# Optimization experiments

Hardware: AMD Instinct MI355X
Metric: run time of the kernel (lower is better)

## Reference

```python
import jax, jax.numpy as jnp
import numpy as np

N = 100000          # nodes
E = 1600000         # edges (before self-loops)
D_IN = 128          # graph.x feature dim
D_HID = 8           # hidden_dim = output_dim = 8 (hard-coded in __init__)
NUM_MASK = 10000    # int(0.1 * N), _mask_rate = 0.1
ATT_SLOPE = 0.2     # GATConv attention LeakyReLU slope
ACT_SLOPE = 0.01    # F.leaky_relu default slope


def setup_inputs() -> dict:
    key = jax.random.key(0)
    ks = jax.random.split(key, 16)
    x = jax.random.normal(ks[0], (N, D_IN), dtype=jnp.float32)
    edge_index = jax.random.randint(ks[1], (2, E), 0, N, dtype=jnp.int32)
    mask_nodes = jax.random.permutation(ks[2], N)[:NUM_MASK].astype(jnp.int32)
    s = lambda k, shape: jax.random.normal(k, shape, dtype=jnp.float32) * 0.1
    return {
        "x": x,
        "edge_index": edge_index,
        "mask_nodes": mask_nodes,
        "enc_mask_token": jnp.zeros((1, D_IN), dtype=jnp.float32),
        "enc_W": s(ks[3], (D_HID, D_IN)),
        "enc_a_src": s(ks[4], (D_HID,)),
        "enc_a_dst": s(ks[5], (D_HID,)),
        "enc_b": s(ks[6], (D_HID,)),
        "e2d_W": s(ks[7], (D_HID, D_HID)),
        "dec_W": s(ks[8], (D_IN, D_HID)),
        "dec_a_src": s(ks[9], (D_IN,)),
        "dec_a_dst": s(ks[10], (D_IN,)),
        "dec_b": s(ks[11], (D_IN,)),
    }


def gat_conv(x, W, a_src, a_dst, b, src, dst, n_nodes):
    """PyG GATConv, heads=1 (self-loops already appended to src/dst)."""
    h = x @ W.T                                  # [N, out]
    alpha_src = h @ a_src                        # [N]
    alpha_dst = h @ a_dst                        # [N]
    e = jax.nn.leaky_relu(alpha_src[src] + alpha_dst[dst], ATT_SLOPE)  # [E]
    # numerically-stable segment softmax over incoming edges per dst node
    m = jax.ops.segment_max(e, dst, num_segments=n_nodes)
    ex = jnp.exp(e - m[dst])
    denom = jax.ops.segment_sum(ex, dst, num_segments=n_nodes)
    alpha = ex / denom[dst]                      # [E]
    out = jax.ops.segment_sum(alpha[:, None] * h[src], dst, num_segments=n_nodes)
    return out + b


def reference(x, edge_index, mask_nodes, enc_mask_token,
              enc_W, enc_a_src, enc_a_dst, enc_b,
              e2d_W, dec_W, dec_a_src, dec_a_dst, dec_b):
    n = x.shape[0]
    # GATConv adds self-loops internally
    loops = jnp.arange(n, dtype=edge_index.dtype)
    src = jnp.concatenate([edge_index[0], loops])
    dst = jnp.concatenate([edge_index[1], loops])

    # encoding_mask_noise: out_x[mask]=0 then += enc_mask_token -> set to token
    use_x = x.at[mask_nodes].set(enc_mask_token[0])

    # encoder: GATConv(input_dim -> 8) + leaky_relu
    enc_rep = jax.nn.leaky_relu(
        gat_conv(use_x, enc_W, enc_a_src, enc_a_dst, enc_b, src, dst, n), ACT_SLOPE)

    rep = enc_rep @ e2d_W.T
    rep = rep.at[mask_nodes].set(0.0)            # re-mask before decoding

    # decoder: GATConv(8 -> input_dim) + leaky_relu
    recon = jax.nn.leaky_relu(
        gat_conv(rep, dec_W, dec_a_src, dec_a_dst, dec_b, src, dst, n), ACT_SLOPE)

    # cosine reconstruction loss on masked nodes (torch eps = 1e-8)
    x_init = x[mask_nodes]
    x_rec = recon[mask_nodes]
    eps = jnp.float32(1e-8)
    na = jnp.maximum(jnp.linalg.norm(x_rec, axis=-1), eps)
    nb = jnp.maximum(jnp.linalg.norm(x_init, axis=-1), eps)
    cos = jnp.sum(x_rec * x_init, axis=-1) / (na * nb)
    loss = 1.0 - jnp.mean(cos)
    return loss, enc_rep
```

## Files before the change

### kernel.cpp

```cpp
#include <hip/hip_runtime.h>

#define N_NODES 100000
#define N_EDGES 1600000
#define D_IN    128
#define D_H     8
#define N_MASK  10000

#define TS      256
#define NTE     391
#define CAPB    5760
#define TSD     64
#define NTD     157
#define CAPD    1536
#define NB_NODE 196
#define EPB     2048
#define NB_BKT  782

__device__ __forceinline__ float lrelu(float v, float s){ return v > 0.f ? v : s*v; }

__device__ __forceinline__ float wave_sum(float v){
#pragma unroll
  for (int o = 32; o > 0; o >>= 1) v += __shfl_xor(v, o, 64);
  return v;
}

__global__ void k_init(int* __restrict__ mask_slot, int* __restrict__ gcur_enc,
                       int* __restrict__ gcur_dec, float* __restrict__ cos_sum,
                       int* __restrict__ ticket){
  int i = blockIdx.x*blockDim.x + threadIdx.x;
  if (i < N_NODES) mask_slot[i] = -1;
  if (i < NTE) gcur_enc[i] = 0;
  if (i < NTD) gcur_dec[i] = 0;
  if (i == 0){ cos_sum[0] = 0.f; ticket[0] = 0; }
}

__global__ void k_ms(const int* __restrict__ mask_nodes, int* __restrict__ mask_slot,
                     const float* __restrict__ Wd, const float* __restrict__ a_src,
                     float* __restrict__ vvec){
  int i = blockIdx.x*blockDim.x + threadIdx.x;
  if (i < N_MASK) mask_slot[mask_nodes[i]] = i;
  if (blockIdx.x == 0 && threadIdx.x < D_H){
    float s = 0.f;
    for (int j = 0; j < D_IN; ++j) s += a_src[j] * Wd[j*D_H + threadIdx.x];
    vvec[threadIdx.x] = s;
  }
}

__global__ void __launch_bounds__(512) k_pre(
    const float* __restrict__ x, const float* __restrict__ token,
    const float* __restrict__ W, const float* __restrict__ a_src,
    const float* __restrict__ a_dst, const int* __restrict__ mask_slot,
    const int* __restrict__ ei,
    float* __restrict__ h1, float* __restrict__ as1, float* __restrict__ ad1,
    int* __restrict__ gcur_enc, int* __restrict__ gcur_dec,
    unsigned* __restrict__ be, unsigned* __restrict__ bd){
  __shared__ int smem[1104];
  if (blockIdx.x < NB_NODE){
    float* Ws = (float*)smem;
    float* sa = Ws + D_H*D_IN;
    float* sd = sa + D_H;
    for (int t = threadIdx.x; t < D_H*D_IN; t += 512) Ws[t] = W[t];
    if (threadIdx.x < D_H)            sa[threadIdx.x] = a_src[threadIdx.x];
    else if (threadIdx.x < 2*D_H)     sd[threadIdx.x - D_H] = a_dst[threadIdx.x - D_H];
    __syncthreads();
    int wid = blockIdx.x*512 + threadIdx.x;
    if (wid >= N_NODES) return;
    const float* row = (mask_slot[wid] >= 0) ? token : (x + (size_t)wid*D_IN);
    float acc[D_H];
#pragma unroll
    for (int j = 0; j < D_H; ++j) acc[j] = 0.f;
#pragma unroll 8
    for (int i = 0; i < D_IN/4; ++i){
      float4 xc = *(const float4*)(row + 4*i);
#pragma unroll
      for (int j = 0; j < D_H; ++j){
        float4 wv = *(const float4*)(Ws + j*D_IN + 4*i);
        acc[j] += xc.x*wv.x + xc.y*wv.y + xc.z*wv.z + xc.w*wv.w;
      }
    }
    float as = 0.f, ad = 0.f;
#pragma unroll
    for (int j = 0; j < D_H; ++j){ as += acc[j]*sa[j]; ad += acc[j]*sd[j]; }
    float4* hp = (float4*)(h1 + (size_t)wid*D_H);
    hp[0] = make_float4(acc[0], acc[1], acc[2], acc[3]);
    hp[1] = make_float4(acc[4], acc[5], acc[6], acc[7]);
    as1[wid] = as; ad1[wid] = ad;
  } else {
    int* h_enc    = smem;
    int* base_enc = h_enc + NTE;
    int* h_dec    = base_enc + NTE;
    int* base_dec = h_dec + NTD;
    int tid = threadIdx.x;
    if (tid < NTE) h_enc[tid] = 0;
    if (tid < NTD) h_dec[tid] = 0;
    __syncthreads();
    int t0 = (blockIdx.x - NB_NODE)*EPB;
    int s[4], d[4], sl[4];
#pragma unroll
    for (int k = 0; k < 4; ++k){
      int t = t0 + tid + k*512;
      s[k] = -1;
      if (t < N_EDGES){
        s[k] = ei[t]; d[k] = ei[N_EDGES + t];
        sl[k] = mask_slot[d[k]];
        atomicAdd(&h_enc[d[k] >> 8], 1);
        if (sl[k] >= 0) atomicAdd(&h_dec[sl[k] >> 6], 1);
      }
    }
    __syncthreads();
    if (tid < NTE){ base_enc[tid] = atomicAdd(&gcur_enc[tid], h_enc[tid]); h_enc[tid] = 0; }
    if (tid < NTD){ base_dec[tid] = atomicAdd(&gcur_dec[tid], h_dec[tid]); h_dec[tid] = 0; }
    __syncthreads();
#pragma unroll
    for (int k = 0; k < 4; ++k){
      if (s[k] >= 0){
        int b = d[k] >> 8, loc = d[k] & 255;
        int idx = base_enc[b] + atomicAdd(&h_enc[b], 1);
        if (idx < CAPB) be[(size_t)b*CAPB + idx] = ((unsigned)s[k] << 8) | (unsigned)loc;
        if (sl[k] >= 0){
          int bs = sl[k] >> 6, locs = sl[k] & 63;
          int i2 = base_dec[bs] + atomicAdd(&h_dec[bs], 1);
          if (i2 < CAPD) bd[(size_t)bs*CAPD + i2] = ((unsigned)s[k] << 6) | (unsigned)locs;
        }
      }
    }
  }
}

__global__ void __launch_bounds__(512) k_agg_enc(const unsigned* __restrict__ be,
                          const int* __restrict__ gcur_enc,
                          const float* __restrict__ as1, const float* __restrict__ ad1,
                          const float* __restrict__ h1,
                          const float* __restrict__ enc_b, const float* __restrict__ e2dW,
                          const int* __restrict__ mask_slot, const float* __restrict__ v,
                          float* __restrict__ out_rep, float* __restrict__ rep,
                          float* __restrict__ ex2){
  __shared__ unsigned sorted[CAPB];
  __shared__ int hist[TS], off[TS], cur[TS];
  __shared__ float lad[TS];
  __shared__ float comb[TS*9];
  int tau = blockIdx.x, tid = threadIdx.x;
  int gb = tau*TS;
  if (tid < TS){
    hist[tid] = 0;
    int g = gb + tid; lad[tid] = (g < N_NODES) ? ad1[g] : 0.f;
  }
  __syncthreads();
  int n = min(gcur_enc[tau], CAPB);
  const unsigned* bb = be + (size_t)tau*CAPB;
  for (int i = tid; i < n; i += 512) atomicAdd(&hist[bb[i] & 255], 1);
  __syncthreads();
  if (tid < TS) off[tid] = hist[tid];
  __syncthreads();
#pragma unroll
  for (int s2 = 1; s2 < TS; s2 <<= 1){
    int vv = 0;
    if (tid < TS && tid >= s2) vv = off[tid - s2];
    __syncthreads();
    if (tid < TS) off[tid] += vv;
    __syncthreads();
  }
  if (tid < TS) cur[tid] = off[tid] - hist[tid];
  __syncthreads();
  for (int i = tid; i < n; i += 512){
    unsigned w = bb[i];
    int pos = atomicAdd(&cur[w & 255], 1);
    sorted[pos] = w;
  }
  __syncthreads();
  int c = tid & 255, half = tid >> 8;
  int start = off[c] - hist[c], deg = hist[c];
  int mid = start + ((deg + 1) >> 1), end = start + deg;
  int k0 = half ? mid : start, k1 = half ? end : mid;
  float adv = lad[c];
  float acc[9];
#pragma unroll
  for (int j = 0; j < 9; ++j) acc[j] = 0.f;
  auto edge1 = [&](unsigned w){
    int s = w >> 8;
    float as = as1[s];
    float4 ha = *(const float4*)(h1 + (size_t)s*D_H);
    float4 hb = *(const float4*)(h1 + (size_t)s*D_H + 4);
    float ex = __expf(lrelu(as + adv, 0.2f));
    acc[0] += ex*ha.x; acc[1] += ex*ha.y; acc[2] += ex*ha.z; acc[3] += ex*ha.w;
    acc[4] += ex*hb.x; acc[5] += ex*hb.y; acc[6] += ex*hb.z; acc[7] += ex*hb.w;
    acc[8] += ex;
  };
  int k = k0;
  for (; k + 4 <= k1; k += 4){
    unsigned w0 = sorted[k], w1 = sorted[k+1], w2 = sorted[k+2], w3 = sorted[k+3];
    int s0 = w0 >> 8, s1 = w1 >> 8, s2 = w2 >> 8, s3 = w3 >> 8;
    float a0 = as1[s0], a1 = as1[s1], a2 = as1[s2], a3 = as1[s3];
    float4 h0a = *(const float4*)(h1 + (size_t)s0*D_H), h0b = *(const float4*)(h1 + (size_t)s0*D_H + 4);
    float4 h1a = *(const float4*)(h1 + (size_t)s1*D_H), h1b = *(const float4*)(h1 + (size_t)s1*D_H + 4);
    float4 h2a = *(const float4*)(h1 + (size_t)s2*D_H), h2b = *(const float4*)(h1 + (size_t)s2*D_H + 4);
    float4 h3a = *(const float4*)(h1 + (size_t)s3*D_H), h3b = *(const float4*)(h1 + (size_t)s3*D_H + 4);
    float e0 = __expf(lrelu(a0 + adv, 0.2f));
    float e1 = __expf(lrelu(a1 + adv, 0.2f));
    float e2 = __expf(lrelu(a2 + adv, 0.2f));
    float e3 = __expf(lrelu(a3 + adv, 0.2f));
    acc[0] += e0*h0a.x + e1*h1a.x + e2*h2a.x + e3*h3a.x;
    acc[1] += e0*h0a.y + e1*h1a.y + e2*h2a.y + e3*h3a.y;
    acc[2] += e0*h0a.z + e1*h1a.z + e2*h2a.z + e3*h3a.z;
    acc[3] += e0*h0a.w + e1*h1a.w + e2*h2a.w + e3*h3a.w;
    acc[4] += e0*h0b.x + e1*h1b.x + e2*h2b.x + e3*h3b.x;
    acc[5] += e0*h0b.y + e1*h1b.y + e2*h2b.y + e3*h3b.y;
    acc[6] += e0*h0b.z + e1*h1b.z + e2*h2b.z + e3*h3b.z;
    acc[7] += e0*h0b.w + e1*h1b.w + e2*h2b.w + e3*h3b.w;
    acc[8] += e0 + e1 + e2 + e3;
  }
  for (; k < k1; ++k) edge1(sorted[k]);
  if (half){
#pragma unroll
    for (int j = 0; j < 9; ++j) comb[c*9 + j] = acc[j];
  }
  __syncthreads();
  if (!half){
    int i = gb + c;
    if (i < N_NODES){
#pragma unroll
      for (int j = 0; j < 9; ++j) acc[j] += comb[c*9 + j];
      {
        float exs = __expf(lrelu(as1[i] + adv, 0.2f));
        float4 ha = *(const float4*)(h1 + (size_t)i*D_H);
        float4 hb = *(const float4*)(h1 + (size_t)i*D_H + 4);
        acc[0] += exs*ha.x; acc[1] += exs*ha.y; acc[2] += exs*ha.z; acc[3] += exs*ha.w;
        acc[4] += exs*hb.x; acc[5] += exs*hb.y; acc[6] += exs*hb.z; acc[7] += exs*hb.w;
        acc[8] += exs;
      }
      float inv = 1.0f / acc[8];
      float er[D_H];
#pragma unroll
      for (int j = 0; j < D_H; ++j){
        er[j] = lrelu(acc[j]*inv + enc_b[j], 0.01f);
        out_rep[(size_t)i*D_H + j] = er[j];
      }
      bool masked = mask_slot[i] >= 0;
      float as = 0.f;
      float rv[D_H];
#pragma unroll
      for (int kk = 0; kk < D_H; ++kk){
        float t = 0.f;
#pragma unroll
        for (int j = 0; j < D_H; ++j) t += er[j]*e2dW[kk*D_H + j];
        t = masked ? 0.f : t;
        rv[kk] = t;
        as += t * v[kk];
      }
      float4* rp = (float4*)(rep + (size_t)i*D_H);
      rp[0] = make_float4(rv[0], rv[1], rv[2], rv[3]);
      rp[1] = make_float4(rv[4], rv[5], rv[6], rv[7]);
      ex2[i] = __expf(lrelu(as, 0.2f));
    }
  }
}

__global__ void __launch_bounds__(512) k_agg_dec(const unsigned* __restrict__ bd,
                          const int* __restrict__ gcur_dec,
                          const float* __restrict__ ex2, const float* __restrict__ rep,
                          const float* __restrict__ Wd, const float* __restrict__ dec_b,
                          const int* __restrict__ mask_nodes, const float* __restrict__ x,
                          float* __restrict__ cos_sum, int* __restrict__ ticket,
                          float* __restrict__ out){
  __shared__ unsigned sorted[CAPD];
  __shared__ int hist[TSD], off[TSD], cur[TSD];
  __shared__ float comb[TSD*9];
  __shared__ float Wt[D_H*D_IN];
  __shared__ float wsum[8];
  int sg = blockIdx.x, tid = threadIdx.x;
  if (tid < TSD) hist[tid] = 0;
  for (int t = tid; t < D_H*D_IN; t += 512) Wt[(t & 7)*D_IN + (t >> 3)] = Wd[t];
  __syncthreads();
  int n = min(gcur_dec[sg], CAPD);
  const unsigned* bb = bd + (size_t)sg*CAPD;
  for (int i = tid; i < n; i += 512) atomicAdd(&hist[bb[i] & 63], 1);
  __syncthreads();
  if (tid < TSD) off[tid] = hist[tid];
  __syncthreads();
#pragma unroll
  for (int s2 = 1; s2 < TSD; s2 <<= 1){
    int vv = 0;
    if (tid < TSD && tid >= s2) vv = off[tid - s2];
    __syncthreads();
    if (tid < TSD) off[tid] += vv;
    __syncthreads();
  }
  if (tid < TSD) cur[tid] = off[tid] - hist[tid];
  __syncthreads();
  for (int i = tid; i < n; i += 512){
    unsigned w = bb[i];
    int pos = atomicAdd(&cur[w & 63], 1);
    sorted[pos] = w;
  }
  __syncthreads();
  int c = tid >> 3, part = tid & 7;
  int start = off[c] - hist[c], deg = hist[c], end = start + deg;
  float acc[9];
#pragma unroll
  for (int j = 0; j < 9; ++j) acc[j] = 0.f;
  int k = start + part;
  for (; k + 8 < end; k += 16){
    unsigned w0 = sorted[k], w1 = sorted[k+8];
    int sA = w0 >> 6, sB = w1 >> 6;
    float eA = ex2[sA], eB = ex2[sB];
    float4 raA = *(const float4*)(rep + (size_t)sA*D_H);
    float4 rbA = *(const float4*)(rep + (size_t)sA*D_H + 4);
    float4 raB = *(const float4*)(rep + (size_t)sB*D_H);
    float4 rbB = *(const float4*)(rep + (size_t)sB*D_H + 4);
    acc[0] += eA*raA.x; acc[1] += eA*raA.y; acc[2] += eA*raA.z; acc[3] += eA*raA.w;
    acc[4] += eA*rbA.x; acc[5] += eA*rbA.y; acc[6] += eA*rbA.z; acc[7] += eA*rbA.w;
    acc[8] += eA;
    acc[0] += eB*raB.x; acc[1] += eB*raB.y; acc[2] += eB*raB.z; acc[3] += eB*raB.w;
    acc[4] += eB*rbB.x; acc[5] += eB*rbB.y; acc[6] += eB*rbB.z; acc[7] += eB*rbB.w;
    acc[8] += eB;
  }
  if (k < end){
    unsigned w = sorted[k];
    int s = w >> 6;
    float E = ex2[s];
    float4 ra = *(const float4*)(rep + (size_t)s*D_H);
    float4 rb = *(const float4*)(rep + (size_t)s*D_H + 4);
    acc[0] += E*ra.x; acc[1] += E*ra.y; acc[2] += E*ra.z; acc[3] += E*ra.w;
    acc[4] += E*rb.x; acc[5] += E*rb.y; acc[6] += E*rb.z; acc[7] += E*rb.w;
    acc[8] += E;
  }
#pragma unroll
  for (int j = 0; j < 9; ++j){
    acc[j] += __shfl_xor(acc[j], 1, 64);
    acc[j] += __shfl_xor(acc[j], 2, 64);
    acc[j] += __shfl_xor(acc[j], 4, 64);
  }
  if (part == 0){
    acc[8] += 1.0f;
#pragma unroll
    for (int j = 0; j < 9; ++j) comb[c*9 + j] = acc[j];
  }
  __syncthreads();
  int wv = tid >> 6, lane = tid & 63;
  float accv = 0.f;
  for (int sl = wv; sl < TSD; sl += 8){
    int slot = sg*TSD + sl;
    if (slot >= N_MASK) break;
    const float* a = comb + sl*9;
    float inv = 1.0f / a[8];
    int node = mask_nodes[slot];
    float dot = 0.f, na = 0.f, nb = 0.f;
#pragma unroll
    for (int hh = 0; hh < 2; ++hh){
      int f = lane + 64*hh;
      float r = dec_b[f];
#pragma unroll
      for (int kk = 0; kk < D_H; ++kk) r += a[kk]*inv*Wt[kk*D_IN + f];
      r = lrelu(r, 0.01f);
      float xi = x[(size_t)node*D_IN + f];
      dot += r*xi; na += r*r; nb += xi*xi;
    }
    dot = wave_sum(dot); na = wave_sum(na); nb = wave_sum(nb);
    if (lane == 0) accv += dot / (fmaxf(sqrtf(na), 1e-8f)*fmaxf(sqrtf(nb), 1e-8f));
  }
  if (lane == 0) wsum[wv] = accv;
  __syncthreads();
  if (tid == 0){
    float b = 0.f;
#pragma unroll
    for (int q = 0; q < 8; ++q) b += wsum[q];
    atomicAdd(cos_sum, b);
    __threadfence();
    int t = atomicAdd(ticket, 1);
    if (t == gridDim.x - 1){
      float cc = atomicAdd(cos_sum, 0.0f);
      out[0] = 1.0f - cc / (float)N_MASK;
    }
  }
}

extern "C" void kernel_launch(void* const* d_in, const int* in_sizes, int n_in,
                              void* d_out, int out_size, void* d_ws, size_t ws_size,
                              hipStream_t stream){
  const float* x          = (const float*)d_in[0];
  const int*   ei         = (const int*)  d_in[1];
  const int*   mask_nodes = (const int*)  d_in[2];
  const float* token      = (const float*)d_in[3];
  const float* enc_W      = (const float*)d_in[4];
  const float* enc_as     = (const float*)d_in[5];
  const float* enc_ad     = (const float*)d_in[6];
  const float* enc_b      = (const float*)d_in[7];
  const float* e2d_W      = (const float*)d_in[8];
  const float* dec_W      = (const float*)d_in[9];
  const float* dec_as     = (const float*)d_in[10];
  const float* dec_b      = (const float*)d_in[12];
  float* out = (float*)d_out;

  char* w = (char*)d_ws;
  size_t off = 0;
  auto alloc = [&](size_t bytes)->char*{ char* p = w + off; off += (bytes + 255)/256*256; return p; };
  int*   gcur_enc = (int*)  alloc(NTE*4);
  int*   gcur_dec = (int*)  alloc(NTD*4);
  float* cos_sum  = (float*)alloc(4);
  int*   ticket   = (int*)  alloc(4);
  int*      mask_slot = (int*)     alloc((size_t)N_NODES*4);
  unsigned* be        = (unsigned*)alloc((size_t)NTE*CAPB*4);
  unsigned* bd        = (unsigned*)alloc((size_t)NTD*CAPD*4);
  float*    h1        = (float*)   alloc((size_t)N_NODES*D_H*4);
  float*    as1       = (float*)   alloc((size_t)N_NODES*4);
  float*    ad1       = (float*)   alloc((size_t)N_NODES*4);
  float*    rep       = (float*)   alloc((size_t)N_NODES*D_H*4);
  float*    ex2       = (float*)   alloc((size_t)N_NODES*4);
  float*    vvec      = (float*)   alloc(64);

  k_init    <<<(N_NODES + 511)/512, 512, 0, stream>>>(mask_slot, gcur_enc, gcur_dec, cos_sum, ticket);
  k_ms      <<<(N_MASK + 255)/256, 256, 0, stream>>>(mask_nodes, mask_slot, dec_W, dec_as, vvec);
  k_pre     <<<NB_NODE + NB_BKT, 512, 0, stream>>>(x, token, enc_W, enc_as, enc_ad, mask_slot,
                                                   ei, h1, as1, ad1, gcur_enc, gcur_dec, be, bd);
  k_agg_enc <<<NTE, 512, 0, stream>>>(be, gcur_enc, as1, ad1, h1, enc_b, e2d_W, mask_slot,
                                      vvec, out + 1, rep, ex2);
  k_agg_dec <<<NTD, 512, 0, stream>>>(bd, gcur_dec, ex2, rep, dec_W, dec_b, mask_nodes, x,
                                      cos_sum, ticket, out);
}
```

Before: 90.97 us.

## Build decoder buckets from sorted encoder buckets and use four threads per node

```diff
diff --git a/kernel.cpp b/kernel.cpp
--- a/kernel.cpp
+++ b/kernel.cpp
@@ -46,14 +46,13 @@
   }
 }
 
-__global__ void __launch_bounds__(512) k_pre(
+__global__ void __launch_bounds__(512, 8) k_pre(
     const float* __restrict__ x, const float* __restrict__ token,
     const float* __restrict__ W, const float* __restrict__ a_src,
     const float* __restrict__ a_dst, const int* __restrict__ mask_slot,
     const int* __restrict__ ei,
     float* __restrict__ h1, float* __restrict__ as1, float* __restrict__ ad1,
-    int* __restrict__ gcur_enc, int* __restrict__ gcur_dec,
-    unsigned* __restrict__ be, unsigned* __restrict__ bd){
+    int* __restrict__ gcur_enc, unsigned* __restrict__ be){
   __shared__ int smem[1104];
   if (blockIdx.x < NB_NODE){
     float* Ws = (float*)smem;
@@ -88,28 +87,22 @@
   } else {
     int* h_enc    = smem;
     int* base_enc = h_enc + NTE;
-    int* h_dec    = base_enc + NTE;
-    int* base_dec = h_dec + NTD;
     int tid = threadIdx.x;
     if (tid < NTE) h_enc[tid] = 0;
-    if (tid < NTD) h_dec[tid] = 0;
     __syncthreads();
     int t0 = (blockIdx.x - NB_NODE)*EPB;
-    int s[4], d[4], sl[4];
+    int s[4], d[4];
 #pragma unroll
     for (int k = 0; k < 4; ++k){
       int t = t0 + tid + k*512;
       s[k] = -1;
       if (t < N_EDGES){
         s[k] = ei[t]; d[k] = ei[N_EDGES + t];
-        sl[k] = mask_slot[d[k]];
         atomicAdd(&h_enc[d[k] >> 8], 1);
-        if (sl[k] >= 0) atomicAdd(&h_dec[sl[k] >> 6], 1);
       }
     }
     __syncthreads();
     if (tid < NTE){ base_enc[tid] = atomicAdd(&gcur_enc[tid], h_enc[tid]); h_enc[tid] = 0; }
-    if (tid < NTD){ base_dec[tid] = atomicAdd(&gcur_dec[tid], h_dec[tid]); h_dec[tid] = 0; }
     __syncthreads();
 #pragma unroll
     for (int k = 0; k < 4; ++k){
@@ -117,38 +110,36 @@
         int b = d[k] >> 8, loc = d[k] & 255;
         int idx = base_enc[b] + atomicAdd(&h_enc[b], 1);
         if (idx < CAPB) be[(size_t)b*CAPB + idx] = ((unsigned)s[k] << 8) | (unsigned)loc;
-        if (sl[k] >= 0){
-          int bs = sl[k] >> 6, locs = sl[k] & 63;
-          int i2 = base_dec[bs] + atomicAdd(&h_dec[bs], 1);
-          if (i2 < CAPD) bd[(size_t)bs*CAPD + i2] = ((unsigned)s[k] << 6) | (unsigned)locs;
-        }
       }
     }
   }
 }
 
-__global__ void __launch_bounds__(512) k_agg_enc(const unsigned* __restrict__ be,
+__global__ void __launch_bounds__(1024) k_agg_enc(const unsigned* __restrict__ be,
                           const int* __restrict__ gcur_enc,
                           const float* __restrict__ as1, const float* __restrict__ ad1,
                           const float* __restrict__ h1,
                           const float* __restrict__ enc_b, const float* __restrict__ e2dW,
                           const int* __restrict__ mask_slot, const float* __restrict__ v,
+                          int* __restrict__ gcur_dec, unsigned* __restrict__ bd,
                           float* __restrict__ out_rep, float* __restrict__ rep,
                           float* __restrict__ ex2){
   __shared__ unsigned sorted[CAPB];
   __shared__ int hist[TS], off[TS], cur[TS];
   __shared__ float lad[TS];
-  __shared__ float comb[TS*9];
+  __shared__ int msl[TS];
   int tau = blockIdx.x, tid = threadIdx.x;
   int gb = tau*TS;
   if (tid < TS){
     hist[tid] = 0;
-    int g = gb + tid; lad[tid] = (g < N_NODES) ? ad1[g] : 0.f;
+    int g = gb + tid;
+    lad[tid] = (g < N_NODES) ? ad1[g] : 0.f;
+    msl[tid] = (g < N_NODES) ? mask_slot[g] : -1;
   }
   __syncthreads();
   int n = min(gcur_enc[tau], CAPB);
   const unsigned* bb = be + (size_t)tau*CAPB;
-  for (int i = tid; i < n; i += 512) atomicAdd(&hist[bb[i] & 255], 1);
+  for (int i = tid; i < n; i += 1024) atomicAdd(&hist[bb[i] & 255], 1);
   __syncthreads();
   if (tid < TS) off[tid] = hist[tid];
   __syncthreads();
@@ -162,21 +153,35 @@
   }
   if (tid < TS) cur[tid] = off[tid] - hist[tid];
   __syncthreads();
-  for (int i = tid; i < n; i += 512){
+  for (int i = tid; i < n; i += 1024){
     unsigned w = bb[i];
     int pos = atomicAdd(&cur[w & 255], 1);
     sorted[pos] = w;
   }
   __syncthreads();
-  int c = tid & 255, half = tid >> 8;
-  int start = off[c] - hist[c], deg = hist[c];
-  int mid = start + ((deg + 1) >> 1), end = start + deg;
-  int k0 = half ? mid : start, k1 = half ? end : mid;
+  int c = tid >> 2, part = tid & 3;
+  int start = off[c] - hist[c], deg = hist[c], end = start + deg;
   float adv = lad[c];
   float acc[9];
 #pragma unroll
   for (int j = 0; j < 9; ++j) acc[j] = 0.f;
-  auto edge1 = [&](unsigned w){
+  int k = start + part;
+  for (; k + 4 < end; k += 8){
+    unsigned w0 = sorted[k], w1 = sorted[k+4];
+    int sA = w0 >> 8, sB = w1 >> 8;
+    float aA = as1[sA], aB = as1[sB];
+    float4 hAa = *(const float4*)(h1 + (size_t)sA*D_H), hAb = *(const float4*)(h1 + (size_t)sA*D_H + 4);
+    float4 hBa = *(const float4*)(h1 + (size_t)sB*D_H), hBb = *(const float4*)(h1 + (size_t)sB*D_H + 4);
+    float eA = __expf(lrelu(aA + adv, 0.2f));
+    float eB = __expf(lrelu(aB + adv, 0.2f));
+    acc[0] += eA*hAa.x + eB*hBa.x; acc[1] += eA*hAa.y + eB*hBa.y;
+    acc[2] += eA*hAa.z + eB*hBa.z; acc[3] += eA*hAa.w + eB*hBa.w;
+    acc[4] += eA*hAb.x + eB*hBb.x; acc[5] += eA*hAb.y + eB*hBb.y;
+    acc[6] += eA*hAb.z + eB*hBb.z; acc[7] += eA*hAb.w + eB*hBb.w;
+    acc[8] += eA + eB;
+  }
+  if (k < end){
+    unsigned w = sorted[k];
     int s = w >> 8;
     float as = as1[s];
     float4 ha = *(const float4*)(h1 + (size_t)s*D_H);
@@ -185,49 +190,33 @@
     acc[0] += ex*ha.x; acc[1] += ex*ha.y; acc[2] += ex*ha.z; acc[3] += ex*ha.w;
     acc[4] += ex*hb.x; acc[5] += ex*hb.y; acc[6] += ex*hb.z; acc[7] += ex*hb.w;
     acc[8] += ex;
-  };
-  int k = k0;
-  for (; k + 4 <= k1; k += 4){
-    unsigned w0 = sorted[k], w1 = sorted[k+1], w2 = sorted[k+2], w3 = sorted[k+3];
-    int s0 = w0 >> 8, s1 = w1 >> 8, s2 = w2 >> 8, s3 = w3 >> 8;
-    float a0 = as1[s0], a1 = as1[s1], a2 = as1[s2], a3 = as1[s3];
-    float4 h0a = *(const float4*)(h1 + (size_t)s0*D_H), h0b = *(const float4*)(h1 + (size_t)s0*D_H + 4);
-    float4 h1a = *(const float4*)(h1 + (size_t)s1*D_H), h1b = *(const float4*)(h1 + (size_t)s1*D_H + 4);
-    float4 h2a = *(const float4*)(h1 + (size_t)s2*D_H), h2b = *(const float4*)(h1 + (size_t)s2*D_H + 4);
-    float4 h3a = *(const float4*)(h1 + (size_t)s3*D_H), h3b = *(const float4*)(h1 + (size_t)s3*D_H + 4);
-    float e0 = __expf(lrelu(a0 + adv, 0.2f));
-    float e1 = __expf(lrelu(a1 + adv, 0.2f));
-    float e2 = __expf(lrelu(a2 + adv, 0.2f));
-    float e3 = __expf(lrelu(a3 + adv, 0.2f));
-    acc[0] += e0*h0a.x + e1*h1a.x + e2*h2a.x + e3*h3a.x;
-    acc[1] += e0*h0a.y + e1*h1a.y + e2*h2a.y + e3*h3a.y;
-    acc[2] += e0*h0a.z + e1*h1a.z + e2*h2a.z + e3*h3a.z;
-    acc[3] += e0*h0a.w + e1*h1a.w + e2*h2a.w + e3*h3a.w;
-    acc[4] += e0*h0b.x + e1*h1b.x + e2*h2b.x + e3*h3b.x;
-    acc[5] += e0*h0b.y + e1*h1b.y + e2*h2b.y + e3*h3b.y;
-    acc[6] += e0*h0b.z + e1*h1b.z + e2*h2b.z + e3*h3b.z;
-    acc[7] += e0*h0b.w + e1*h1b.w + e2*h2b.w + e3*h3b.w;
-    acc[8] += e0 + e1 + e2 + e3;
-  }
-  for (; k < k1; ++k) edge1(sorted[k]);
-  if (half){
-#pragma unroll
-    for (int j = 0; j < 9; ++j) comb[c*9 + j] = acc[j];
-  }
-  __syncthreads();
-  if (!half){
+  }
+#pragma unroll
+  for (int j = 0; j < 9; ++j){
+    acc[j] += __shfl_xor(acc[j], 1, 64);
+    acc[j] += __shfl_xor(acc[j], 2, 64);
+  }
+  int slot = msl[c];
+  if (slot >= 0 && deg > 0){
+    int sg = slot >> 6;
+    unsigned locs = (unsigned)(slot & 63);
+    int base = 0;
+    if (part == 0) base = atomicAdd(&gcur_dec[sg], deg);
+    base = __shfl(base, (int)((tid & 63) & ~3), 64);
+    for (int kk = start + part; kk < end; kk += 4){
+      int pos = base + (kk - start);
+      if (pos < CAPD) bd[(size_t)sg*CAPD + pos] = ((sorted[kk] >> 8) << 6) | locs;
+    }
+  }
+  if (part == 0){
     int i = gb + c;
     if (i < N_NODES){
-#pragma unroll
-      for (int j = 0; j < 9; ++j) acc[j] += comb[c*9 + j];
-      {
-        float exs = __expf(lrelu(as1[i] + adv, 0.2f));
-        float4 ha = *(const float4*)(h1 + (size_t)i*D_H);
-        float4 hb = *(const float4*)(h1 + (size_t)i*D_H + 4);
-        acc[0] += exs*ha.x; acc[1] += exs*ha.y; acc[2] += exs*ha.z; acc[3] += exs*ha.w;
-        acc[4] += exs*hb.x; acc[5] += exs*hb.y; acc[6] += exs*hb.z; acc[7] += exs*hb.w;
-        acc[8] += exs;
-      }
+      float exs = __expf(lrelu(as1[i] + adv, 0.2f));
+      float4 ha = *(const float4*)(h1 + (size_t)i*D_H);
+      float4 hb = *(const float4*)(h1 + (size_t)i*D_H + 4);
+      acc[0] += exs*ha.x; acc[1] += exs*ha.y; acc[2] += exs*ha.z; acc[3] += exs*ha.w;
+      acc[4] += exs*hb.x; acc[5] += exs*hb.y; acc[6] += exs*hb.z; acc[7] += exs*hb.w;
+      acc[8] += exs;
       float inv = 1.0f / acc[8];
       float er[D_H];
 #pragma unroll
@@ -235,7 +224,7 @@
         er[j] = lrelu(acc[j]*inv + enc_b[j], 0.01f);
         out_rep[(size_t)i*D_H + j] = er[j];
       }
-      bool masked = mask_slot[i] >= 0;
+      bool masked = slot >= 0;
       float as = 0.f;
       float rv[D_H];
 #pragma unroll
@@ -411,9 +400,9 @@
   k_init    <<<(N_NODES + 511)/512, 512, 0, stream>>>(mask_slot, gcur_enc, gcur_dec, cos_sum, ticket);
   k_ms      <<<(N_MASK + 255)/256, 256, 0, stream>>>(mask_nodes, mask_slot, dec_W, dec_as, vvec);
   k_pre     <<<NB_NODE + NB_BKT, 512, 0, stream>>>(x, token, enc_W, enc_as, enc_ad, mask_slot,
-                                                   ei, h1, as1, ad1, gcur_enc, gcur_dec, be, bd);
-  k_agg_enc <<<NTE, 512, 0, stream>>>(be, gcur_enc, as1, ad1, h1, enc_b, e2d_W, mask_slot,
-                                      vvec, out + 1, rep, ex2);
+                                                   ei, h1, as1, ad1, gcur_enc, be);
+  k_agg_enc <<<NTE, 1024, 0, stream>>>(be, gcur_enc, as1, ad1, h1, enc_b, e2d_W, mask_slot,
+                                       vvec, gcur_dec, bd, out + 1, rep, ex2);
   k_agg_dec <<<NTD, 512, 0, stream>>>(bd, gcur_dec, ex2, rep, dec_W, dec_b, mask_nodes, x,
                                       cos_sum, ticket, out);
 }
```

Result: slower. 98.39 us (+8.2%).
